# Kernel tuning notes

Measured on AMD Instinct MI355X. Metric: run time of the kernel, lower is better.

Reference implementation:

```python
import jax, jax.numpy as jnp
import numpy as np

B, H, S, D = 4, 16, 2048, 64

def setup_inputs() -> dict:
    key = jax.random.key(0)
    k1, k2, k3 = jax.random.split(key, 3)
    query = jax.random.normal(k1, (B, H, S, D), dtype=jnp.float32)
    key_t = jax.random.normal(k2, (B, H, S, D), dtype=jnp.float32)
    value = jax.random.normal(k3, (B, H, S, D), dtype=jnp.float32)
    return {"query": query, "key": key_t, "value": value}

def reference(query, key, value):
    # scale = 1/sqrt(sqrt(D)) applied to BOTH q and k -> effective 1/sqrt(D) on logits
    d = query.shape[-1]
    scale = 1.0 / jnp.sqrt(jnp.sqrt(jnp.asarray(d, query.dtype)))
    q = query * scale
    k = key * scale
    # [B,H,L,S] attention logits
    attn = jnp.einsum('bhld,bhsd->bhls', q, k)
    L, Skv = q.shape[-2], k.shape[-2]
    causal = jnp.tril(jnp.ones((L, Skv), dtype=bool))  # lower-triangular keep-mask
    attn = jnp.where(causal, attn, jnp.asarray(-jnp.inf, attn.dtype))
    attn = jax.nn.softmax(attn, axis=-1)
    # dropout_p == 0.0 -> no dropout
    return jnp.einsum('bhls,bhsd->bhld', attn, value)
```

## Files before the change

### kernel.cpp

```cpp
#include <hip/hip_runtime.h>


typedef short bf16x4 __attribute__((ext_vector_type(4)));
typedef short bf16x8 __attribute__((ext_vector_type(8)));
typedef float f32x16 __attribute__((ext_vector_type(16)));

#define S_LEN 2048
#define D_DIM 64
#define KVB 64
#define KSTR 68
#define VSTR 68
#define SC_LOG2E 0.18033688011112042f

__device__ __forceinline__ unsigned pk2(float lo, float hi) {
    return __builtin_amdgcn_perm(__builtin_bit_cast(unsigned, hi),
                                 __builtin_bit_cast(unsigned, lo), 0x07060302u);
}

__device__ __forceinline__ bf16x8 ldfrag(const short* p) {
    bf16x4 lo = *(const bf16x4*)(p);
    bf16x4 hi = *(const bf16x4*)(p + 4);
    bf16x8 r;
    r[0] = lo[0]; r[1] = lo[1]; r[2] = lo[2]; r[3] = lo[3];
    r[4] = hi[0]; r[5] = hi[1]; r[6] = hi[2]; r[7] = hi[3];
    return r;
}

__device__ __forceinline__ bf16x8 mk8(unsigned u0, unsigned u1, unsigned u2, unsigned u3) {
    union { unsigned u[4]; bf16x8 v; } r;
    r.u[0] = u0; r.u[1] = u1; r.u[2] = u2; r.u[3] = u3;
    return r.v;
}

__device__ __forceinline__ f32x16 zero16() {
    return f32x16{0.f,0.f,0.f,0.f,0.f,0.f,0.f,0.f,
                  0.f,0.f,0.f,0.f,0.f,0.f,0.f,0.f};
}

__global__ __launch_bounds__(256, 2) void fattn_kernel(
    const float* __restrict__ Q, const float* __restrict__ K,
    const float* __restrict__ V, float* __restrict__ O)
{
    __shared__ short Kl[2][KVB * KSTR];
    __shared__ short Vt[2][D_DIM * VSTR];

    const int t    = threadIdx.x;
    const int wid  = t >> 6;
    const int lane = t & 63;
    const int h    = lane >> 5;
    const int l31  = lane & 31;

    const int flat  = blockIdx.x;
    const int halfg = flat >> 8;
    const int r     = flat & 255;
    const int xcd   = r & 7;
    const int rr    = r >> 3;
    const int bh    = xcd * 8 + (rr & 7);
    const int slot  = rr >> 3;
    const int ip    = halfg ? (7 - slot) : slot;

    const int ntb = 32 - 2 * ip;
    const int nta = 2 * ip + 2;
    const int q0b = (15 - ip) * 128;
    const int q0a = ip * 128;

    const size_t base = (size_t)bh * (S_LEN * D_DIM);
    const float* Qh = Q + base;
    const float* Kh = K + base;
    const float* Vh = V + base;
    float*       Oh = O + base;

    const int skv = t >> 2;
    const int sd  = (t & 3) * 16;
    const int vkv = (t & 31) * 2;
    const int vdd = (t >> 5) * 8;
    const int sT = vkv >> 5, sm = (vkv >> 3) & 3, sh = (vkv >> 2) & 1, st = vkv & 3;
    const int vslot = 32 * sT + 16 * (sm >> 1) + 8 * sh + 4 * (sm & 1) + st;

    bf16x8 aqB[4], aqA[4];
    {
        const float* qp = Qh + (size_t)(q0b + 32 * wid + l31) * D_DIM;
        #pragma unroll
        for (int s = 0; s < 4; ++s) {
            const int d0 = 16 * s + 8 * h;
            float4 a = *(const float4*)(qp + d0);
            float4 b = *(const float4*)(qp + d0 + 4);
            aqB[s] = mk8(pk2(a.x * SC_LOG2E, a.y * SC_LOG2E),
                         pk2(a.z * SC_LOG2E, a.w * SC_LOG2E),
                         pk2(b.x * SC_LOG2E, b.y * SC_LOG2E),
                         pk2(b.z * SC_LOG2E, b.w * SC_LOG2E));
        }
    }
    {
        const float* qp = Qh + (size_t)(q0a + 32 * wid + l31) * D_DIM;
        #pragma unroll
        for (int s = 0; s < 4; ++s) {
            const int d0 = 16 * s + 8 * h;
            float4 a = *(const float4*)(qp + d0);
            float4 b = *(const float4*)(qp + d0 + 4);
            aqA[s] = mk8(pk2(a.x * SC_LOG2E, a.y * SC_LOG2E),
                         pk2(a.z * SC_LOG2E, a.w * SC_LOG2E),
                         pk2(b.x * SC_LOG2E, b.y * SC_LOG2E),
                         pk2(b.z * SC_LOG2E, b.w * SC_LOG2E));
        }
    }

    f32x16 oB[2], oA[2];
    oB[0] = zero16(); oB[1] = zero16();
    oA[0] = zero16(); oA[1] = zero16();
    float lpB = 0.f, lpA = 0.f;
    const int qBl = q0b + 32 * wid + l31;
    const int qAl = q0a + 32 * wid + l31;

    float4 kr0, kr1, kr2, kr3, vr0, vr1, vr2, vr3;

#define PREFETCH(tl) do {                                                     \
        const float* kp_ = Kh + (size_t)((tl) * KVB + skv) * D_DIM + sd;      \
        kr0 = *(const float4*)(kp_);     kr1 = *(const float4*)(kp_ + 4);     \
        kr2 = *(const float4*)(kp_ + 8); kr3 = *(const float4*)(kp_ + 12);    \
        const float* vp_ = Vh + (size_t)((tl) * KVB + vkv) * D_DIM + vdd;     \
        vr0 = *(const float4*)(vp_);         vr1 = *(const float4*)(vp_ + 4); \
        vr2 = *(const float4*)(vp_ + D_DIM); vr3 = *(const float4*)(vp_ + D_DIM + 4); \
    } while (0)

#define STAGE(KB, VB) do {                                                    \
        short* kd_ = (KB) + skv * KSTR + sd;                                  \
        *(uint2*)(kd_)      = make_uint2(pk2(kr0.x, kr0.y), pk2(kr0.z, kr0.w)); \
        *(uint2*)(kd_ + 4)  = make_uint2(pk2(kr1.x, kr1.y), pk2(kr1.z, kr1.w)); \
        *(uint2*)(kd_ + 8)  = make_uint2(pk2(kr2.x, kr2.y), pk2(kr2.z, kr2.w)); \
        *(uint2*)(kd_ + 12) = make_uint2(pk2(kr3.x, kr3.y), pk2(kr3.z, kr3.w)); \
        short* vd_ = (VB) + vslot;                                            \
        *(unsigned*)(vd_ + (vdd + 0) * VSTR) = pk2(vr0.x, vr2.x);             \
        *(unsigned*)(vd_ + (vdd + 1) * VSTR) = pk2(vr0.y, vr2.y);             \
        *(unsigned*)(vd_ + (vdd + 2) * VSTR) = pk2(vr0.z, vr2.z);             \
        *(unsigned*)(vd_ + (vdd + 3) * VSTR) = pk2(vr0.w, vr2.w);             \
        *(unsigned*)(vd_ + (vdd + 4) * VSTR) = pk2(vr1.x, vr3.x);             \
        *(unsigned*)(vd_ + (vdd + 5) * VSTR) = pk2(vr1.y, vr3.y);             \
        *(unsigned*)(vd_ + (vdd + 6) * VSTR) = pk2(vr1.z, vr3.z);             \
        *(unsigned*)(vd_ + (vdd + 7) * VSTR) = pk2(vr1.w, vr3.w);             \
    } while (0)

    PREFETCH(0);
    STAGE(Kl[0], Vt[0]);
    if (ntb > 1) PREFETCH(1);
    __syncthreads();

    #pragma unroll 1
    for (int kt = 0; kt < ntb; ++kt) {
        const int cur = kt & 1;
        const short* Kb = Kl[cur];
        const short* Vb = Vt[cur];
        const bool doA = (kt < nta);

        if (kt + 1 < ntb) {
            STAGE(Kl[cur ^ 1], Vt[cur ^ 1]);
            if (kt + 2 < ntb) PREFETCH(kt + 2);
        }

        unsigned pbB[16], pbA[16];
        __builtin_amdgcn_s_setprio(1);

        #pragma unroll
        for (int T = 0; T < 2; ++T) {
            const short* kp = &Kb[(32 * T + l31) * KSTR + 8 * h];
            const bf16x8 kf0 = ldfrag(kp);
            const bf16x8 kf1 = ldfrag(kp + 16);
            const bf16x8 kf2 = ldfrag(kp + 32);
            const bf16x8 kf3 = ldfrag(kp + 48);
            const int kvb = 64 * kt + 32 * T;

            {
                f32x16 z = zero16();
                z = __builtin_amdgcn_mfma_f32_32x32x16_bf16(kf0, aqB[0], z, 0, 0, 0);
                z = __builtin_amdgcn_mfma_f32_32x32x16_bf16(kf1, aqB[1], z, 0, 0, 0);
                z = __builtin_amdgcn_mfma_f32_32x32x16_bf16(kf2, aqB[2], z, 0, 0, 0);
                z = __builtin_amdgcn_mfma_f32_32x32x16_bf16(kf3, aqB[3], z, 0, 0, 0);
                const bool mB = (64 * kt + 63 > q0b + 32 * wid);
                float e[16];
                #pragma unroll
                for (int rg = 0; rg < 16; ++rg) {
                    float x = z[rg];
                    if (mB && (kvb + (rg & 3) + 8 * (rg >> 2) + 4 * h > qBl))
                        x = -__builtin_inff();
                    e[rg] = __builtin_amdgcn_exp2f(x);
                }
                lpB += (((e[0]+e[1])+(e[2]+e[3])) + ((e[4]+e[5])+(e[6]+e[7])))
                     + (((e[8]+e[9])+(e[10]+e[11])) + ((e[12]+e[13])+(e[14]+e[15])));
                #pragma unroll
                for (int k2 = 0; k2 < 8; ++k2)
                    pbB[8 * T + k2] = pk2(e[2 * k2], e[2 * k2 + 1]);
            }
            if (doA) {
                f32x16 z = zero16();
                z = __builtin_amdgcn_mfma_f32_32x32x16_bf16(kf0, aqA[0], z, 0, 0, 0);
                z = __builtin_amdgcn_mfma_f32_32x32x16_bf16(kf1, aqA[1], z, 0, 0, 0);
                z = __builtin_amdgcn_mfma_f32_32x32x16_bf16(kf2, aqA[2], z, 0, 0, 0);
                z = __builtin_amdgcn_mfma_f32_32x32x16_bf16(kf3, aqA[3], z, 0, 0, 0);
                const bool mA = (64 * kt + 63 > q0a + 32 * wid);
                float e[16];
                #pragma unroll
                for (int rg = 0; rg < 16; ++rg) {
                    float x = z[rg];
                    if (mA && (kvb + (rg & 3) + 8 * (rg >> 2) + 4 * h > qAl))
                        x = -__builtin_inff();
                    e[rg] = __builtin_amdgcn_exp2f(x);
                }
                lpA += (((e[0]+e[1])+(e[2]+e[3])) + ((e[4]+e[5])+(e[6]+e[7])))
                     + (((e[8]+e[9])+(e[10]+e[11])) + ((e[12]+e[13])+(e[14]+e[15])));
                #pragma unroll
                for (int k2 = 0; k2 < 8; ++k2)
                    pbA[8 * T + k2] = pk2(e[2 * k2], e[2 * k2 + 1]);
            }
        }

        #pragma unroll
        for (int DT = 0; DT < 2; ++DT) {
            const short* vp = &Vb[(32 * DT + l31) * VSTR + 8 * h];
            #pragma unroll
            for (int s = 0; s < 4; ++s) {
                const bf16x8 vf = ldfrag(vp + 16 * s);
                const bf16x8 pfB = mk8(pbB[4*s], pbB[4*s+1], pbB[4*s+2], pbB[4*s+3]);
                oB[DT] = __builtin_amdgcn_mfma_f32_32x32x16_bf16(pfB, vf, oB[DT], 0, 0, 0);
                if (doA) {
                    const bf16x8 pfA = mk8(pbA[4*s], pbA[4*s+1], pbA[4*s+2], pbA[4*s+3]);
                    oA[DT] = __builtin_amdgcn_mfma_f32_32x32x16_bf16(pfA, vf, oA[DT], 0, 0, 0);
                }
            }
        }
        __builtin_amdgcn_s_setprio(0);

        __syncthreads();
    }

    lpB += __shfl_xor(lpB, 32, 64);
    lpA += __shfl_xor(lpA, 32, 64);
    #pragma unroll
    for (int rg = 0; rg < 16; ++rg) {
        const int qrow = (rg & 3) + 8 * (rg >> 2) + 4 * h;
        const float invB = 1.0f / __shfl(lpB, qrow, 64);
        const float invA = 1.0f / __shfl(lpA, qrow, 64);
        float* opB = Oh + (size_t)(q0b + 32 * wid + qrow) * D_DIM + l31;
        float* opA = Oh + (size_t)(q0a + 32 * wid + qrow) * D_DIM + l31;
        opB[0]  = oB[0][rg] * invB;
        opB[32] = oB[1][rg] * invB;
        opA[0]  = oA[0][rg] * invA;
        opA[32] = oA[1][rg] * invA;
    }
}

extern "C" void kernel_launch(void* const* d_in, const int* in_sizes, int n_in,
                              void* d_out, int out_size, void* d_ws, size_t ws_size,
                              hipStream_t stream) {
    const float* Q = (const float*)d_in[0];
    const float* K = (const float*)d_in[1];
    const float* V = (const float*)d_in[2];
    float*       O = (float*)d_out;
    dim3 grid(512);
    fattn_kernel<<<grid, 256, 0, stream>>>(Q, K, V, O);
}
```

Before: 173.8 us.

## Use 512-thread blocks with one 256-row query tile per block

Each block now owns one contiguous 256-row query tile, spread over 8 waves of 32 rows each, in place of two paired 128-row tiles across 4 waves. Load balance comes from pairing j and 7-j across the two block rounds. K and V staging is split so that V staging overlaps the first half-tile compute. Waves skip key tiles past their causal diagonal, and only the diagonal half-tile is masked. Register pressure per thread drops, which allows higher occupancy, but waves inside a block now have unequal work and still wait at every block barrier.

```diff
diff --git a/kernel.cpp b/kernel.cpp
--- a/kernel.cpp
+++ b/kernel.cpp
@@ -37,7 +37,7 @@
                   0.f,0.f,0.f,0.f,0.f,0.f,0.f,0.f};
 }
 
-__global__ __launch_bounds__(256, 2) void fattn_kernel(
+__global__ __launch_bounds__(512, 4) void fattn_kernel(
     const float* __restrict__ Q, const float* __restrict__ K,
     const float* __restrict__ V, float* __restrict__ O)
 {
@@ -51,18 +51,18 @@
     const int l31  = lane & 31;
 
     const int flat  = blockIdx.x;
-    const int halfg = flat >> 8;
+    const int round = flat >> 8;
     const int r     = flat & 255;
     const int xcd   = r & 7;
     const int rr    = r >> 3;
     const int bh    = xcd * 8 + (rr & 7);
     const int slot  = rr >> 3;
-    const int ip    = halfg ? (7 - slot) : slot;
-
-    const int ntb = 32 - 2 * ip;
-    const int nta = 2 * ip + 2;
-    const int q0b = (15 - ip) * 128;
-    const int q0a = ip * 128;
+    const int j     = round ? (7 - slot) : slot;
+
+    const int q0     = j * 256;
+    const int nt     = 4 * (j + 1);
+    const int qbase  = q0 + 32 * wid;
+    const int ktlast = 4 * j + (wid >> 1);
 
     const size_t base = (size_t)bh * (S_LEN * D_DIM);
     const float* Qh = Q + base;
@@ -70,181 +70,140 @@
     const float* Vh = V + base;
     float*       Oh = O + base;
 
-    const int skv = t >> 2;
-    const int sd  = (t & 3) * 16;
+    const int skv = t >> 3;
+    const int sd  = (t & 7) * 8;
     const int vkv = (t & 31) * 2;
-    const int vdd = (t >> 5) * 8;
+    const int vdd = (t >> 5) * 4;
     const int sT = vkv >> 5, sm = (vkv >> 3) & 3, sh = (vkv >> 2) & 1, st = vkv & 3;
     const int vslot = 32 * sT + 16 * (sm >> 1) + 8 * sh + 4 * (sm & 1) + st;
 
-    bf16x8 aqB[4], aqA[4];
+    bf16x8 aq[4];
     {
-        const float* qp = Qh + (size_t)(q0b + 32 * wid + l31) * D_DIM;
+        const float* qp = Qh + (size_t)(qbase + l31) * D_DIM;
         #pragma unroll
         for (int s = 0; s < 4; ++s) {
             const int d0 = 16 * s + 8 * h;
             float4 a = *(const float4*)(qp + d0);
             float4 b = *(const float4*)(qp + d0 + 4);
-            aqB[s] = mk8(pk2(a.x * SC_LOG2E, a.y * SC_LOG2E),
-                         pk2(a.z * SC_LOG2E, a.w * SC_LOG2E),
-                         pk2(b.x * SC_LOG2E, b.y * SC_LOG2E),
-                         pk2(b.z * SC_LOG2E, b.w * SC_LOG2E));
+            aq[s] = mk8(pk2(a.x * SC_LOG2E, a.y * SC_LOG2E),
+                        pk2(a.z * SC_LOG2E, a.w * SC_LOG2E),
+                        pk2(b.x * SC_LOG2E, b.y * SC_LOG2E),
+                        pk2(b.z * SC_LOG2E, b.w * SC_LOG2E));
         }
     }
-    {
-        const float* qp = Qh + (size_t)(q0a + 32 * wid + l31) * D_DIM;
-        #pragma unroll
-        for (int s = 0; s < 4; ++s) {
-            const int d0 = 16 * s + 8 * h;
-            float4 a = *(const float4*)(qp + d0);
-            float4 b = *(const float4*)(qp + d0 + 4);
-            aqA[s] = mk8(pk2(a.x * SC_LOG2E, a.y * SC_LOG2E),
-                         pk2(a.z * SC_LOG2E, a.w * SC_LOG2E),
-                         pk2(b.x * SC_LOG2E, b.y * SC_LOG2E),
-                         pk2(b.z * SC_LOG2E, b.w * SC_LOG2E));
-        }
-    }
-
-    f32x16 oB[2], oA[2];
-    oB[0] = zero16(); oB[1] = zero16();
-    oA[0] = zero16(); oA[1] = zero16();
-    float lpB = 0.f, lpA = 0.f;
-    const int qBl = q0b + 32 * wid + l31;
-    const int qAl = q0a + 32 * wid + l31;
-
-    float4 kr0, kr1, kr2, kr3, vr0, vr1, vr2, vr3;
-
-#define PREFETCH(tl) do {                                                     \
+
+    f32x16 o0 = zero16(), o1 = zero16();
+    float lpx0 = 0.f, lpx1 = 0.f;
+    const int thr = l31 - 4 * h;
+
+    float4 kr0, kr1, vr0, vr1;
+
+#define PREFK(tl) do {                                                        \
         const float* kp_ = Kh + (size_t)((tl) * KVB + skv) * D_DIM + sd;      \
-        kr0 = *(const float4*)(kp_);     kr1 = *(const float4*)(kp_ + 4);     \
-        kr2 = *(const float4*)(kp_ + 8); kr3 = *(const float4*)(kp_ + 12);    \
+        kr0 = *(const float4*)(kp_); kr1 = *(const float4*)(kp_ + 4);         \
+    } while (0)
+#define PREFV(tl) do {                                                        \
         const float* vp_ = Vh + (size_t)((tl) * KVB + vkv) * D_DIM + vdd;     \
-        vr0 = *(const float4*)(vp_);         vr1 = *(const float4*)(vp_ + 4); \
-        vr2 = *(const float4*)(vp_ + D_DIM); vr3 = *(const float4*)(vp_ + D_DIM + 4); \
-    } while (0)
-
-#define STAGE(KB, VB) do {                                                    \
+        vr0 = *(const float4*)(vp_); vr1 = *(const float4*)(vp_ + D_DIM);     \
+    } while (0)
+#define STAGEK(KB) do {                                                       \
         short* kd_ = (KB) + skv * KSTR + sd;                                  \
-        *(uint2*)(kd_)      = make_uint2(pk2(kr0.x, kr0.y), pk2(kr0.z, kr0.w)); \
-        *(uint2*)(kd_ + 4)  = make_uint2(pk2(kr1.x, kr1.y), pk2(kr1.z, kr1.w)); \
-        *(uint2*)(kd_ + 8)  = make_uint2(pk2(kr2.x, kr2.y), pk2(kr2.z, kr2.w)); \
-        *(uint2*)(kd_ + 12) = make_uint2(pk2(kr3.x, kr3.y), pk2(kr3.z, kr3.w)); \
+        *(uint2*)(kd_)     = make_uint2(pk2(kr0.x, kr0.y), pk2(kr0.z, kr0.w));\
+        *(uint2*)(kd_ + 4) = make_uint2(pk2(kr1.x, kr1.y), pk2(kr1.z, kr1.w));\
+    } while (0)
+#define STAGEV(VB) do {                                                       \
         short* vd_ = (VB) + vslot;                                            \
-        *(unsigned*)(vd_ + (vdd + 0) * VSTR) = pk2(vr0.x, vr2.x);             \
-        *(unsigned*)(vd_ + (vdd + 1) * VSTR) = pk2(vr0.y, vr2.y);             \
-        *(unsigned*)(vd_ + (vdd + 2) * VSTR) = pk2(vr0.z, vr2.z);             \
-        *(unsigned*)(vd_ + (vdd + 3) * VSTR) = pk2(vr0.w, vr2.w);             \
-        *(unsigned*)(vd_ + (vdd + 4) * VSTR) = pk2(vr1.x, vr3.x);             \
-        *(unsigned*)(vd_ + (vdd + 5) * VSTR) = pk2(vr1.y, vr3.y);             \
-        *(unsigned*)(vd_ + (vdd + 6) * VSTR) = pk2(vr1.z, vr3.z);             \
-        *(unsigned*)(vd_ + (vdd + 7) * VSTR) = pk2(vr1.w, vr3.w);             \
-    } while (0)
-
-    PREFETCH(0);
-    STAGE(Kl[0], Vt[0]);
-    if (ntb > 1) PREFETCH(1);
+        *(unsigned*)(vd_ + (vdd + 0) * VSTR) = pk2(vr0.x, vr1.x);             \
+        *(unsigned*)(vd_ + (vdd + 1) * VSTR) = pk2(vr0.y, vr1.y);             \
+        *(unsigned*)(vd_ + (vdd + 2) * VSTR) = pk2(vr0.z, vr1.z);             \
+        *(unsigned*)(vd_ + (vdd + 3) * VSTR) = pk2(vr0.w, vr1.w);             \
+    } while (0)
+
+#define QK_EXP_T(Tofs, msk) do {                                              \
+        const short* kp_ = &Kb[((Tofs) + l31) * KSTR + 8 * h];                \
+        const bf16x8 kf0 = ldfrag(kp_);                                       \
+        const bf16x8 kf1 = ldfrag(kp_ + 16);                                  \
+        const bf16x8 kf2 = ldfrag(kp_ + 32);                                  \
+        const bf16x8 kf3 = ldfrag(kp_ + 48);                                  \
+        f32x16 z = zero16();                                                  \
+        z = __builtin_amdgcn_mfma_f32_32x32x16_bf16(kf0, aq[0], z, 0, 0, 0);  \
+        z = __builtin_amdgcn_mfma_f32_32x32x16_bf16(kf1, aq[1], z, 0, 0, 0);  \
+        z = __builtin_amdgcn_mfma_f32_32x32x16_bf16(kf2, aq[2], z, 0, 0, 0);  \
+        z = __builtin_amdgcn_mfma_f32_32x32x16_bf16(kf3, aq[3], z, 0, 0, 0);  \
+        _Pragma("unroll")                                                     \
+        for (int k2 = 0; k2 < 8; ++k2) {                                      \
+            const int i0 = ((2*k2) & 3) + 8 * ((2*k2) >> 2);                  \
+            float x0 = z[2*k2], x1 = z[2*k2+1];                               \
+            if (msk) {                                                        \
+                if (i0 > thr)     x0 = -__builtin_inff();                     \
+                if (i0 + 1 > thr) x1 = -__builtin_inff();                     \
+            }                                                                 \
+            const float e0 = __builtin_amdgcn_exp2f(x0);                      \
+            const float e1 = __builtin_amdgcn_exp2f(x1);                      \
+            if (k2 < 4) lpx0 += e0 + e1; else lpx1 += e0 + e1;                \
+            pb[k2] = pk2(e0, e1);                                             \
+        }                                                                     \
+    } while (0)
+
+#define PV2(sbase) do {                                                       \
+        _Pragma("unroll")                                                     \
+        for (int sg = 0; sg < 2; ++sg) {                                      \
+            const int co = 16 * ((sbase) + sg) + 8 * h;                       \
+            const bf16x8 pf = mk8(pb[4*sg], pb[4*sg+1], pb[4*sg+2], pb[4*sg+3]); \
+            const bf16x8 vf0 = ldfrag(&Vb[l31 * VSTR + co]);                  \
+            const bf16x8 vf1 = ldfrag(&Vb[(32 + l31) * VSTR + co]);           \
+            o0 = __builtin_amdgcn_mfma_f32_32x32x16_bf16(pf, vf0, o0, 0, 0, 0); \
+            o1 = __builtin_amdgcn_mfma_f32_32x32x16_bf16(pf, vf1, o1, 0, 0, 0); \
+        }                                                                     \
+    } while (0)
+
+    PREFK(0); PREFV(0);
+    STAGEK(Kl[0]); STAGEV(Vt[0]);
+    PREFK(1); PREFV(1);
     __syncthreads();
 
     #pragma unroll 1
-    for (int kt = 0; kt < ntb; ++kt) {
+    for (int kt = 0; kt < nt; ++kt) {
         const int cur = kt & 1;
         const short* Kb = Kl[cur];
         const short* Vb = Vt[cur];
-        const bool doA = (kt < nta);
-
-        if (kt + 1 < ntb) {
-            STAGE(Kl[cur ^ 1], Vt[cur ^ 1]);
-            if (kt + 2 < ntb) PREFETCH(kt + 2);
+        const bool more   = (kt + 1 < nt);
+        const bool active = (kt <= ktlast);
+        const bool diag   = (kt == ktlast);
+
+        if (more) STAGEK(Kl[cur ^ 1]);
+        if (kt + 2 < nt) PREFK(kt + 2);
+
+        unsigned pb[8];
+        if (active) {
+            __builtin_amdgcn_s_setprio(1);
+            QK_EXP_T(0, (diag && !(wid & 1)));
+            PV2(0);
+            __builtin_amdgcn_s_setprio(0);
         }
 
-        unsigned pbB[16], pbA[16];
-        __builtin_amdgcn_s_setprio(1);
-
-        #pragma unroll
-        for (int T = 0; T < 2; ++T) {
-            const short* kp = &Kb[(32 * T + l31) * KSTR + 8 * h];
-            const bf16x8 kf0 = ldfrag(kp);
-            const bf16x8 kf1 = ldfrag(kp + 16);
-            const bf16x8 kf2 = ldfrag(kp + 32);
-            const bf16x8 kf3 = ldfrag(kp + 48);
-            const int kvb = 64 * kt + 32 * T;
-
-            {
-                f32x16 z = zero16();
-                z = __builtin_amdgcn_mfma_f32_32x32x16_bf16(kf0, aqB[0], z, 0, 0, 0);
-                z = __builtin_amdgcn_mfma_f32_32x32x16_bf16(kf1, aqB[1], z, 0, 0, 0);
-                z = __builtin_amdgcn_mfma_f32_32x32x16_bf16(kf2, aqB[2], z, 0, 0, 0);
-                z = __builtin_amdgcn_mfma_f32_32x32x16_bf16(kf3, aqB[3], z, 0, 0, 0);
-                const bool mB = (64 * kt + 63 > q0b + 32 * wid);
-                float e[16];
-                #pragma unroll
-                for (int rg = 0; rg < 16; ++rg) {
-                    float x = z[rg];
-                    if (mB && (kvb + (rg & 3) + 8 * (rg >> 2) + 4 * h > qBl))
-                        x = -__builtin_inff();
-                    e[rg] = __builtin_amdgcn_exp2f(x);
-                }
-                lpB += (((e[0]+e[1])+(e[2]+e[3])) + ((e[4]+e[5])+(e[6]+e[7])))
-                     + (((e[8]+e[9])+(e[10]+e[11])) + ((e[12]+e[13])+(e[14]+e[15])));
-                #pragma unroll
-                for (int k2 = 0; k2 < 8; ++k2)
-                    pbB[8 * T + k2] = pk2(e[2 * k2], e[2 * k2 + 1]);
-            }
-            if (doA) {
-                f32x16 z = zero16();
-                z = __builtin_amdgcn_mfma_f32_32x32x16_bf16(kf0, aqA[0], z, 0, 0, 0);
-                z = __builtin_amdgcn_mfma_f32_32x32x16_bf16(kf1, aqA[1], z, 0, 0, 0);
-                z = __builtin_amdgcn_mfma_f32_32x32x16_bf16(kf2, aqA[2], z, 0, 0, 0);
-                z = __builtin_amdgcn_mfma_f32_32x32x16_bf16(kf3, aqA[3], z, 0, 0, 0);
-                const bool mA = (64 * kt + 63 > q0a + 32 * wid);
-                float e[16];
-                #pragma unroll
-                for (int rg = 0; rg < 16; ++rg) {
-                    float x = z[rg];
-                    if (mA && (kvb + (rg & 3) + 8 * (rg >> 2) + 4 * h > qAl))
-                        x = -__builtin_inff();
-                    e[rg] = __builtin_amdgcn_exp2f(x);
-                }
-                lpA += (((e[0]+e[1])+(e[2]+e[3])) + ((e[4]+e[5])+(e[6]+e[7])))
-                     + (((e[8]+e[9])+(e[10]+e[11])) + ((e[12]+e[13])+(e[14]+e[15])));
-                #pragma unroll
-                for (int k2 = 0; k2 < 8; ++k2)
-                    pbA[8 * T + k2] = pk2(e[2 * k2], e[2 * k2 + 1]);
-            }
+        if (more) STAGEV(Vt[cur ^ 1]);
+        if (kt + 2 < nt) PREFV(kt + 2);
+
+        if (active && !(diag && !(wid & 1))) {
+            __builtin_amdgcn_s_setprio(1);
+            QK_EXP_T(32, (diag && (wid & 1)));
+            PV2(2);
+            __builtin_amdgcn_s_setprio(0);
         }
-
-        #pragma unroll
-        for (int DT = 0; DT < 2; ++DT) {
-            const short* vp = &Vb[(32 * DT + l31) * VSTR + 8 * h];
-            #pragma unroll
-            for (int s = 0; s < 4; ++s) {
-                const bf16x8 vf = ldfrag(vp + 16 * s);
-                const bf16x8 pfB = mk8(pbB[4*s], pbB[4*s+1], pbB[4*s+2], pbB[4*s+3]);
-                oB[DT] = __builtin_amdgcn_mfma_f32_32x32x16_bf16(pfB, vf, oB[DT], 0, 0, 0);
-                if (doA) {
-                    const bf16x8 pfA = mk8(pbA[4*s], pbA[4*s+1], pbA[4*s+2], pbA[4*s+3]);
-                    oA[DT] = __builtin_amdgcn_mfma_f32_32x32x16_bf16(pfA, vf, oA[DT], 0, 0, 0);
-                }
-            }
-        }
-        __builtin_amdgcn_s_setprio(0);
 
         __syncthreads();
     }
 
-    lpB += __shfl_xor(lpB, 32, 64);
-    lpA += __shfl_xor(lpA, 32, 64);
+    float lp = lpx0 + lpx1;
+    lp += __shfl_xor(lp, 32, 64);
     #pragma unroll
     for (int rg = 0; rg < 16; ++rg) {
         const int qrow = (rg & 3) + 8 * (rg >> 2) + 4 * h;
-        const float invB = 1.0f / __shfl(lpB, qrow, 64);
-        const float invA = 1.0f / __shfl(lpA, qrow, 64);
-        float* opB = Oh + (size_t)(q0b + 32 * wid + qrow) * D_DIM + l31;
-        float* opA = Oh + (size_t)(q0a + 32 * wid + qrow) * D_DIM + l31;
-        opB[0]  = oB[0][rg] * invB;
-        opB[32] = oB[1][rg] * invB;
-        opA[0]  = oA[0][rg] * invA;
-        opA[32] = oA[1][rg] * invA;
+        const float inv = 1.0f / __shfl(lp, qrow, 64);
+        float* op = Oh + (size_t)(qbase + qrow) * D_DIM + l31;
+        op[0]  = o0[rg] * inv;
+        op[32] = o1[rg] * inv;
     }
 }
 
@@ -256,5 +215,5 @@
     const float* V = (const float*)d_in[2];
     float*       O = (float*)d_out;
     dim3 grid(512);
-    fattn_kernel<<<grid, 256, 0, stream>>>(Q, K, V, O);
-}
+    fattn_kernel<<<grid, 512, 0, stream>>>(Q, K, V, O);
+}
```

Result: no change. 170.4 us (-2.0%).
